# Kernel tuning notes

Hardware: AMD Instinct MI355X
Metric: run time of the kernel (lower is better)

## Reference

```python
import jax, jax.numpy as jnp
import numpy as np

B, T, C = 4, 2048, 1024
H = 16
D = C // H  # head_dim = 64


def setup_inputs() -> dict:
    key = jax.random.key(0)
    k1, k2, k3, k4, k5 = jax.random.split(key, 5)
    s = 0.02
    return {
        "x": jax.random.normal(k1, (B, T, C), dtype=jnp.float32),
        "W_qkv": jax.random.normal(k2, (C, 3 * C), dtype=jnp.float32) * s,
        "b_qkv": jax.random.normal(k3, (3 * C,), dtype=jnp.float32) * s,
        "W_o": jax.random.normal(k4, (C, C), dtype=jnp.float32) * s,
        "b_o": jax.random.normal(k5, (C,), dtype=jnp.float32) * s,
    }


def reference(x, W_qkv, b_qkv, W_o, b_o):
    b, t, c = x.shape
    scaling = D ** (-0.5)
    qkv = x @ W_qkv + b_qkv                      # [B,T,3C]
    q, k, v = jnp.split(qkv, 3, axis=-1)         # each [B,T,C]
    q = q.reshape(b, t, H, D).transpose(0, 2, 1, 3)  # [B,H,T,D]
    k = k.reshape(b, t, H, D).transpose(0, 2, 1, 3)
    v = v.reshape(b, t, H, D).transpose(0, 2, 1, 3)
    scores = jnp.einsum("bhqd,bhkd->bhqk", q, k) * scaling  # [B,H,T,T]
    mask = jnp.tril(jnp.ones((t, t), dtype=bool))            # causal
    scores = jnp.where(mask[None, None, :, :], scores, -jnp.inf)
    probs = jax.nn.softmax(scores, axis=-1)
    out = jnp.einsum("bhqk,bhkd->bhqd", probs, v)            # [B,H,T,D]
    out = out.transpose(0, 2, 1, 3).reshape(b, t, c)         # [B,T,C]
    return out @ W_o + b_o
```

## Files before the change

### kernel.cpp

```cpp
#include <hip/hip_runtime.h>
#include <hip/hip_bf16.h>

typedef unsigned short ushort_t;
typedef __attribute__((ext_vector_type(8))) short short8;
typedef __attribute__((ext_vector_type(4))) float floatx4;
typedef __attribute__((ext_vector_type(2))) unsigned uint2v;
typedef __attribute__((ext_vector_type(4))) unsigned uint4v;

#define B_ 4
#define T_ 2048
#define C_ 1024
#define H_ 16
#define D_ 64
#define BT_ (B_ * T_)
#define N3C (3 * C_)

#define KSC 0.18033688011112042f

__device__ __forceinline__ ushort_t f2bf(float f) {
    unsigned u = __float_as_uint(f);
    u += 0x7FFF + ((u >> 16) & 1);
    return (ushort_t)(u >> 16);
}
__device__ __forceinline__ unsigned pack2bf(float a, float b) {
    __hip_bfloat162 h = __float22bfloat162_rn(make_float2(a, b));
    return *(unsigned*)&h;
}

__device__ __forceinline__ void gload16(const ushort_t* g, ushort_t* l) {
    __builtin_amdgcn_global_load_lds((const __attribute__((address_space(1))) void*)g,
                                     (__attribute__((address_space(3))) void*)l, 16, 0, 0);
}

__global__ void convert_x_k(const float* __restrict__ xin, ushort_t* __restrict__ xb) {
    size_t i = ((size_t)blockIdx.x * 256 + threadIdx.x) * 8;
    const float* xf = xin + i;
    float4 a = *(const float4*)xf;
    float4 b = *(const float4*)(xf + 4);
    short8 o;
    o[0] = (short)f2bf(a.x); o[1] = (short)f2bf(a.y);
    o[2] = (short)f2bf(a.z); o[3] = (short)f2bf(a.w);
    o[4] = (short)f2bf(b.x); o[5] = (short)f2bf(b.y);
    o[6] = (short)f2bf(b.z); o[7] = (short)f2bf(b.w);
    *(short8*)&xb[i] = o;
}

__global__ void transpose_k(const float* __restrict__ in, ushort_t* __restrict__ out,
                            int R, int Nc) {
    __shared__ ushort_t t[32][33];
    int bc = blockIdx.x * 32;
    int br = blockIdx.y * 32;
    int lx = threadIdx.x & 31, ly = threadIdx.x >> 5;
#pragma unroll
    for (int i = 0; i < 4; ++i) {
        int r = ly + i * 8;
        t[r][lx] = f2bf(in[(size_t)(br + r) * Nc + bc + lx]);
    }
    __syncthreads();
#pragma unroll
    for (int i = 0; i < 4; ++i) {
        int r = ly + i * 8;
        out[(size_t)(bc + r) * R + br + lx] = t[lx][r];
    }
}

__global__ void vtrans_k(const ushort_t* __restrict__ in, ushort_t* __restrict__ out) {
    __shared__ ushort_t t[32][33];
    int bh = blockIdx.z;
    const ushort_t* I = in + (size_t)bh * T_ * D_;
    ushort_t* O = out + (size_t)bh * D_ * T_;
    int bt = blockIdx.x * 32, bd = blockIdx.y * 32;
    int lx = threadIdx.x & 31, ly = threadIdx.x >> 5;
#pragma unroll
    for (int i = 0; i < 4; ++i) {
        int r = ly + i * 8;
        t[r][lx] = I[(size_t)(bt + r) * D_ + bd + lx];
    }
    __syncthreads();
#pragma unroll
    for (int i = 0; i < 4; ++i) {
        int r = ly + i * 8;
        O[(size_t)(bd + r) * T_ + bt + lx] = t[lx][r];
    }
}

template <int MODE>
__launch_bounds__(256)
__global__ void gemm_bt(const ushort_t* __restrict__ A, const ushort_t* __restrict__ Bt,
                        const float* __restrict__ bias, float* __restrict__ Cout,
                        ushort_t* __restrict__ Qo, ushort_t* __restrict__ Ko,
                        ushort_t* __restrict__ Vo, int M, int N, int K) {
    __shared__ __align__(16) ushort_t Alds[128 * 32];
    __shared__ __align__(16) ushort_t Blds[128 * 32];
    int tid = threadIdx.x;
    int wave = tid >> 6, lane = tid & 63;
    int bm = blockIdx.x * 128, bn = blockIdx.y * 128;
    int wr = (wave >> 1) * 64, wc = (wave & 1) * 64;
    int lm = lane & 15, lk = (lane >> 4) * 8, lq = lane >> 4;

    floatx4 acc[4][4] = {};

    int srow = tid >> 2;
    int scol = (tid & 3) * 8;
    const ushort_t* Ab = A + (size_t)(bm + srow) * K + scol;
    const ushort_t* Bb = Bt + (size_t)(bn + srow) * K + scol;
    ushort_t* Al0 = &Alds[wave * 512];
    ushort_t* Al1 = &Alds[2048 + wave * 512];
    ushort_t* Bl0 = &Blds[wave * 512];
    ushort_t* Bl1 = &Blds[2048 + wave * 512];
    size_t rowskip = (size_t)64 * K;

    for (int k0 = 0; k0 < K; k0 += 32) {
        __syncthreads();
        gload16(Ab + k0, Al0);
        gload16(Ab + k0 + rowskip, Al1);
        gload16(Bb + k0, Bl0);
        gload16(Bb + k0 + rowskip, Bl1);
        __syncthreads();
        short8 af[4], bf[4];
#pragma unroll
        for (int i = 0; i < 4; ++i)
            af[i] = *(const short8*)&Alds[(wr + i * 16 + lm) * 32 + lk];
#pragma unroll
        for (int i = 0; i < 4; ++i)
            bf[i] = *(const short8*)&Blds[(wc + i * 16 + lm) * 32 + lk];
#pragma unroll
        for (int mi = 0; mi < 4; ++mi)
#pragma unroll
            for (int ni = 0; ni < 4; ++ni)
                acc[mi][ni] = __builtin_amdgcn_mfma_f32_16x16x32_bf16(
                    af[mi], bf[ni], acc[mi][ni], 0, 0, 0);
    }

#pragma unroll
    for (int mi = 0; mi < 4; ++mi) {
#pragma unroll
        for (int ni = 0; ni < 4; ++ni) {
            int col = bn + wc + ni * 16 + lm;
            float bv = bias[col];
#pragma unroll
            for (int r = 0; r < 4; ++r) {
                int row = bm + wr + mi * 16 + lq * 4 + r;
                float v = acc[mi][ni][r] + bv;
                if (MODE == 0) {
                    Cout[(size_t)row * N + col] = v;
                } else {
                    int b = row >> 11, t = row & (T_ - 1);
                    int which = col >> 10, c = col & (C_ - 1);
                    int h = c >> 6, d = c & 63;
                    int bh = b * H_ + h;
                    size_t idx = ((size_t)bh * T_ + t) * D_ + d;
                    if (which == 0)
                        Qo[idx] = f2bf(v * KSC);
                    else if (which == 1)
                        Ko[idx] = f2bf(v);
                    else
                        Vo[idx] = f2bf(v);
                }
            }
        }
    }
}

__launch_bounds__(256)
__global__ void attn_k(const ushort_t* __restrict__ Q, const ushort_t* __restrict__ K,
                       const ushort_t* __restrict__ Vt, ushort_t* __restrict__ O) {
    __shared__ __align__(16) ushort_t KV[2][2][64 * 64];

    int tid = threadIdx.x, wave = tid >> 6, lane = tid & 63;
    int id = blockIdx.x;
    int xcd = id & 7, j = id >> 3;
    int band = 31 - (j & 31);
    int bh = xcd + 8 * (j >> 5);
    int b = bh >> 4, h = bh & 15;
    int lm = lane & 15, lq = lane >> 4, m7 = lane & 7;

    const ushort_t* Qp = Q + (size_t)bh * T_ * D_;
    const ushort_t* Kp = K + (size_t)bh * T_ * D_;
    const ushort_t* Vp = Vt + (size_t)bh * D_ * T_;
    ushort_t* Ob = O + ((size_t)b * T_) * C_ + h * D_;

    int sr = lane >> 3;
    int sc = (lane & 7) ^ sr;
    const ushort_t* Kst = Kp + (size_t)(wave * 16 + sr) * D_ + sc * 8;
    const ushort_t* Vst = Vp + (size_t)(wave * 16 + sr) * T_ + sc * 8;
    int lds0 = (wave * 2 + 0) * 512;
    int lds1 = (wave * 2 + 1) * 512;

    short8 onesf = {};
    if (lm == 0) {
#pragma unroll
        for (int jj = 0; jj < 8; ++jj) onesf[jj] = (short)0x3F80;
    }

    int m0 = band * 64 + wave * 16;

    short8 qf0 = *(const short8*)&Qp[(size_t)(m0 + lm) * D_ + lq * 8];
    short8 qf1 = *(const short8*)&Qp[(size_t)(m0 + lm) * D_ + 32 + lq * 8];

    floatx4 oacc[5] = {};

    int ntw = band + 1;

    gload16(Kst, &KV[0][0][lds0]);
    gload16(Kst + (size_t)8 * D_, &KV[0][0][lds1]);
    gload16(Vst, &KV[0][1][lds0]);
    gload16(Vst + (size_t)8 * T_, &KV[0][1][lds1]);
    __syncthreads();

    int cur = 0;
    for (int it = 0; it < ntw; ++it) {
        if (it + 1 < ntw) {
            size_t kv0n = (size_t)(it + 1) * 64;
            gload16(Kst + kv0n * D_, &KV[cur ^ 1][0][lds0]);
            gload16(Kst + kv0n * D_ + 8 * D_, &KV[cur ^ 1][0][lds1]);
            gload16(Vst + kv0n, &KV[cur ^ 1][1][lds0]);
            gload16(Vst + kv0n + 8 * T_, &KV[cur ^ 1][1][lds1]);
        }
        const ushort_t* Kb = &KV[cur][0][0];
        const ushort_t* Vb = &KV[cur][1][0];

        short8 kf[4][2], vf[4][2];
#pragma unroll
        for (int nt = 0; nt < 4; ++nt) {
            kf[nt][0] = *(const short8*)&Kb[(nt * 16 + lm) * 64 + ((lq ^ m7) * 8)];
            kf[nt][1] = *(const short8*)&Kb[(nt * 16 + lm) * 64 + (((lq + 4) ^ m7) * 8)];
        }

        floatx4 st[4] = {};
#pragma unroll
        for (int nt = 0; nt < 4; ++nt) {
            st[nt] = __builtin_amdgcn_mfma_f32_16x16x32_bf16(kf[nt][0], qf0, st[nt], 0, 0, 0);
            st[nt] = __builtin_amdgcn_mfma_f32_16x16x32_bf16(kf[nt][1], qf1, st[nt], 0, 0, 0);
        }

#pragma unroll
        for (int dt = 0; dt < 4; ++dt) {
            vf[dt][0] = *(const short8*)&Vb[(dt * 16 + lm) * 64 + ((lq ^ m7) * 8)];
            vf[dt][1] = *(const short8*)&Vb[(dt * 16 + lm) * 64 + (((lq + 4) ^ m7) * 8)];
        }

        int kv0 = it * 64;
        if (it == ntw - 1) {
            int mg = m0 + lm;
#pragma unroll
            for (int nt = 0; nt < 4; ++nt)
#pragma unroll
                for (int r = 0; r < 4; ++r) {
                    int kvg = kv0 + nt * 16 + lq * 4 + r;
                    if (kvg > mg) st[nt][r] = -__builtin_inff();
                }
        }

        unsigned e0 = pack2bf(__builtin_amdgcn_exp2f(st[0][0]), __builtin_amdgcn_exp2f(st[0][1]));
        unsigned e1 = pack2bf(__builtin_amdgcn_exp2f(st[0][2]), __builtin_amdgcn_exp2f(st[0][3]));
        unsigned e2 = pack2bf(__builtin_amdgcn_exp2f(st[1][0]), __builtin_amdgcn_exp2f(st[1][1]));
        unsigned e3 = pack2bf(__builtin_amdgcn_exp2f(st[1][2]), __builtin_amdgcn_exp2f(st[1][3]));
        unsigned e4 = pack2bf(__builtin_amdgcn_exp2f(st[2][0]), __builtin_amdgcn_exp2f(st[2][1]));
        unsigned e5 = pack2bf(__builtin_amdgcn_exp2f(st[2][2]), __builtin_amdgcn_exp2f(st[2][3]));
        unsigned e6 = pack2bf(__builtin_amdgcn_exp2f(st[3][0]), __builtin_amdgcn_exp2f(st[3][1]));
        unsigned e7 = pack2bf(__builtin_amdgcn_exp2f(st[3][2]), __builtin_amdgcn_exp2f(st[3][3]));

        uint2v ra = __builtin_amdgcn_permlane32_swap(e0, e2, false, false);
        uint2v wa = __builtin_amdgcn_permlane16_swap(ra[0], ra[1], false, false);
        uint2v rb = __builtin_amdgcn_permlane32_swap(e1, e3, false, false);
        uint2v wb = __builtin_amdgcn_permlane16_swap(rb[0], rb[1], false, false);
        uint2v rc = __builtin_amdgcn_permlane32_swap(e4, e6, false, false);
        uint2v wc = __builtin_amdgcn_permlane16_swap(rc[0], rc[1], false, false);
        uint2v rd = __builtin_amdgcn_permlane32_swap(e5, e7, false, false);
        uint2v wd = __builtin_amdgcn_permlane16_swap(rd[0], rd[1], false, false);

        short8 pb0 = __builtin_bit_cast(short8, (uint4v){wa[0], wb[0], wa[1], wb[1]});
        short8 pb1 = __builtin_bit_cast(short8, (uint4v){wc[0], wd[0], wc[1], wd[1]});

#pragma unroll
        for (int dt = 0; dt < 4; ++dt) {
            oacc[dt] = __builtin_amdgcn_mfma_f32_16x16x32_bf16(vf[dt][0], pb0, oacc[dt], 0, 0, 0);
            oacc[dt] = __builtin_amdgcn_mfma_f32_16x16x32_bf16(vf[dt][1], pb1, oacc[dt], 0, 0, 0);
        }
        oacc[4] = __builtin_amdgcn_mfma_f32_16x16x32_bf16(onesf, pb0, oacc[4], 0, 0, 0);
        oacc[4] = __builtin_amdgcn_mfma_f32_16x16x32_bf16(onesf, pb1, oacc[4], 0, 0, 0);

        __syncthreads();
        cur ^= 1;
    }

    float li = __shfl(oacc[4][0], lm, 64);
    float inv = 1.0f / li;
    int tg = m0 + lm;
#pragma unroll
    for (int dt = 0; dt < 4; ++dt) {
        uint2 pk;
        pk.x = pack2bf(oacc[dt][0] * inv, oacc[dt][1] * inv);
        pk.y = pack2bf(oacc[dt][2] * inv, oacc[dt][3] * inv);
        *(uint2*)&Ob[(size_t)tg * C_ + dt * 16 + lq * 4] = pk;
    }
}

extern "C" void kernel_launch(void* const* d_in, const int* in_sizes, int n_in,
                              void* d_out, int out_size, void* d_ws, size_t ws_size,
                              hipStream_t stream) {
    const float* x    = (const float*)d_in[0];
    const float* Wqkv = (const float*)d_in[1];
    const float* bqkv = (const float*)d_in[2];
    const float* Wo   = (const float*)d_in[3];
    const float* bo   = (const float*)d_in[4];

    ushort_t* ws = (ushort_t*)d_ws;
    ushort_t* WqkvT = ws;
    ushort_t* WoT   = WqkvT + (size_t)N3C * C_;
    ushort_t* Xb    = WoT + (size_t)C_ * C_;
    ushort_t* Qs    = Xb + (size_t)BT_ * C_;
    ushort_t* Ks    = Qs + (size_t)BT_ * C_;
    ushort_t* Vs    = Ks + (size_t)BT_ * C_;
    ushort_t* Attn  = Vs + (size_t)BT_ * C_;

    convert_x_k<<<BT_ * C_ / (256 * 8), 256, 0, stream>>>(x, Xb);
    transpose_k<<<dim3(N3C / 32, C_ / 32), 256, 0, stream>>>(Wqkv, WqkvT, C_, N3C);
    transpose_k<<<dim3(C_ / 32, C_ / 32), 256, 0, stream>>>(Wo, WoT, C_, C_);
    gemm_bt<1><<<dim3(BT_ / 128, N3C / 128), 256, 0, stream>>>(
        Xb, WqkvT, bqkv, nullptr, Qs, Ks, Attn, BT_, N3C, C_);
    vtrans_k<<<dim3(T_ / 32, D_ / 32, B_ * H_), 256, 0, stream>>>(Attn, Vs);
    attn_k<<<2048, 256, 0, stream>>>(Qs, Ks, Vs, Attn);
    gemm_bt<0><<<dim3(BT_ / 128, C_ / 128), 256, 0, stream>>>(
        Attn, WoT, bo, (float*)d_out, nullptr, nullptr, nullptr, BT_, C_, C_);
}
```

Measured before the change: 278.9 us.

## Fuse prep kernels, double-buffer GEMM LDS, write V transposed, add MFMA priority

Merges the x conversion and the two weight transposes into one launch, and removes the separate V transpose kernel by having the QKV GEMM epilogue write V directly in [bh][d][t] layout. The GEMM main loop now double-buffers its LDS tiles so global-to-LDS loads for the next k-step overlap the current MFMAs, at the cost of twice the LDS. The attention kernel raises wave priority around its MFMA blocks with s_setprio. The transposed V store is strided in t, which may make the epilogue writes less coalesced.

```diff
diff --git a/kernel.cpp b/kernel.cpp
--- a/kernel.cpp
+++ b/kernel.cpp
@@ -32,24 +32,32 @@
                                      (__attribute__((address_space(3))) void*)l, 16, 0, 0);
 }
 
-__global__ void convert_x_k(const float* __restrict__ xin, ushort_t* __restrict__ xb) {
-    size_t i = ((size_t)blockIdx.x * 256 + threadIdx.x) * 8;
-    const float* xf = xin + i;
-    float4 a = *(const float4*)xf;
-    float4 b = *(const float4*)(xf + 4);
-    short8 o;
-    o[0] = (short)f2bf(a.x); o[1] = (short)f2bf(a.y);
-    o[2] = (short)f2bf(a.z); o[3] = (short)f2bf(a.w);
-    o[4] = (short)f2bf(b.x); o[5] = (short)f2bf(b.y);
-    o[6] = (short)f2bf(b.z); o[7] = (short)f2bf(b.w);
-    *(short8*)&xb[i] = o;
-}
-
-__global__ void transpose_k(const float* __restrict__ in, ushort_t* __restrict__ out,
-                            int R, int Nc) {
+__global__ void prep_k(const float* __restrict__ x, ushort_t* __restrict__ xb,
+                       const float* __restrict__ Wqkv, ushort_t* __restrict__ WqkvT,
+                       const float* __restrict__ Wo, ushort_t* __restrict__ WoT) {
     __shared__ ushort_t t[32][33];
-    int bc = blockIdx.x * 32;
-    int br = blockIdx.y * 32;
+    int id = blockIdx.x;
+    if (id < 4096) {
+        size_t i = ((size_t)id * 256 + threadIdx.x) * 8;
+        const float* xf = x + i;
+        float4 a = *(const float4*)xf;
+        float4 b = *(const float4*)(xf + 4);
+        short8 o;
+        o[0] = (short)f2bf(a.x); o[1] = (short)f2bf(a.y);
+        o[2] = (short)f2bf(a.z); o[3] = (short)f2bf(a.w);
+        o[4] = (short)f2bf(b.x); o[5] = (short)f2bf(b.y);
+        o[6] = (short)f2bf(b.z); o[7] = (short)f2bf(b.w);
+        *(short8*)&xb[i] = o;
+        return;
+    }
+    int tt = id - 4096;
+    int bx = tt & 127, by = tt >> 7;
+    const float* in;
+    ushort_t* out;
+    int Nc, bc;
+    if (bx < 96) { in = Wqkv; out = WqkvT; Nc = N3C; bc = bx * 32; }
+    else         { in = Wo;   out = WoT;   Nc = C_;  bc = (bx - 96) * 32; }
+    int br = by * 32;
     int lx = threadIdx.x & 31, ly = threadIdx.x >> 5;
 #pragma unroll
     for (int i = 0; i < 4; ++i) {
@@ -60,27 +68,7 @@
 #pragma unroll
     for (int i = 0; i < 4; ++i) {
         int r = ly + i * 8;
-        out[(size_t)(bc + r) * R + br + lx] = t[lx][r];
-    }
-}
-
-__global__ void vtrans_k(const ushort_t* __restrict__ in, ushort_t* __restrict__ out) {
-    __shared__ ushort_t t[32][33];
-    int bh = blockIdx.z;
-    const ushort_t* I = in + (size_t)bh * T_ * D_;
-    ushort_t* O = out + (size_t)bh * D_ * T_;
-    int bt = blockIdx.x * 32, bd = blockIdx.y * 32;
-    int lx = threadIdx.x & 31, ly = threadIdx.x >> 5;
-#pragma unroll
-    for (int i = 0; i < 4; ++i) {
-        int r = ly + i * 8;
-        t[r][lx] = I[(size_t)(bt + r) * D_ + bd + lx];
-    }
-    __syncthreads();
-#pragma unroll
-    for (int i = 0; i < 4; ++i) {
-        int r = ly + i * 8;
-        O[(size_t)(bd + r) * T_ + bt + lx] = t[lx][r];
+        out[(size_t)(bc + r) * C_ + br + lx] = t[lx][r];
     }
 }
 
@@ -90,8 +78,8 @@
                         const float* __restrict__ bias, float* __restrict__ Cout,
                         ushort_t* __restrict__ Qo, ushort_t* __restrict__ Ko,
                         ushort_t* __restrict__ Vo, int M, int N, int K) {
-    __shared__ __align__(16) ushort_t Alds[128 * 32];
-    __shared__ __align__(16) ushort_t Blds[128 * 32];
+    __shared__ __align__(16) ushort_t Alds[2][128 * 32];
+    __shared__ __align__(16) ushort_t Blds[2][128 * 32];
     int tid = threadIdx.x;
     int wave = tid >> 6, lane = tid & 63;
     int bm = blockIdx.x * 128, bn = blockIdx.y * 128;
@@ -104,32 +92,38 @@
     int scol = (tid & 3) * 8;
     const ushort_t* Ab = A + (size_t)(bm + srow) * K + scol;
     const ushort_t* Bb = Bt + (size_t)(bn + srow) * K + scol;
-    ushort_t* Al0 = &Alds[wave * 512];
-    ushort_t* Al1 = &Alds[2048 + wave * 512];
-    ushort_t* Bl0 = &Blds[wave * 512];
-    ushort_t* Bl1 = &Blds[2048 + wave * 512];
+    int lo0 = wave * 512, lo1 = 2048 + wave * 512;
     size_t rowskip = (size_t)64 * K;
 
+    gload16(Ab, &Alds[0][lo0]);
+    gload16(Ab + rowskip, &Alds[0][lo1]);
+    gload16(Bb, &Blds[0][lo0]);
+    gload16(Bb + rowskip, &Blds[0][lo1]);
+    __syncthreads();
+
+    int cur = 0;
     for (int k0 = 0; k0 < K; k0 += 32) {
-        __syncthreads();
-        gload16(Ab + k0, Al0);
-        gload16(Ab + k0 + rowskip, Al1);
-        gload16(Bb + k0, Bl0);
-        gload16(Bb + k0 + rowskip, Bl1);
-        __syncthreads();
+        if (k0 + 32 < K) {
+            gload16(Ab + k0 + 32, &Alds[cur ^ 1][lo0]);
+            gload16(Ab + k0 + 32 + rowskip, &Alds[cur ^ 1][lo1]);
+            gload16(Bb + k0 + 32, &Blds[cur ^ 1][lo0]);
+            gload16(Bb + k0 + 32 + rowskip, &Blds[cur ^ 1][lo1]);
+        }
         short8 af[4], bf[4];
 #pragma unroll
         for (int i = 0; i < 4; ++i)
-            af[i] = *(const short8*)&Alds[(wr + i * 16 + lm) * 32 + lk];
+            af[i] = *(const short8*)&Alds[cur][(wr + i * 16 + lm) * 32 + lk];
 #pragma unroll
         for (int i = 0; i < 4; ++i)
-            bf[i] = *(const short8*)&Blds[(wc + i * 16 + lm) * 32 + lk];
+            bf[i] = *(const short8*)&Blds[cur][(wc + i * 16 + lm) * 32 + lk];
 #pragma unroll
         for (int mi = 0; mi < 4; ++mi)
 #pragma unroll
             for (int ni = 0; ni < 4; ++ni)
                 acc[mi][ni] = __builtin_amdgcn_mfma_f32_16x16x32_bf16(
                     af[mi], bf[ni], acc[mi][ni], 0, 0, 0);
+        __syncthreads();
+        cur ^= 1;
     }
 
 #pragma unroll
@@ -149,13 +143,12 @@
                     int which = col >> 10, c = col & (C_ - 1);
                     int h = c >> 6, d = c & 63;
                     int bh = b * H_ + h;
-                    size_t idx = ((size_t)bh * T_ + t) * D_ + d;
                     if (which == 0)
-                        Qo[idx] = f2bf(v * KSC);
+                        Qo[((size_t)bh * T_ + t) * D_ + d] = f2bf(v * KSC);
                     else if (which == 1)
-                        Ko[idx] = f2bf(v);
+                        Ko[((size_t)bh * T_ + t) * D_ + d] = f2bf(v);
                     else
-                        Vo[idx] = f2bf(v);
+                        Vo[((size_t)bh * D_ + d) * T_ + t] = f2bf(v);
                 }
             }
         }
@@ -228,11 +221,13 @@
         }
 
         floatx4 st[4] = {};
+        __builtin_amdgcn_s_setprio(1);
 #pragma unroll
         for (int nt = 0; nt < 4; ++nt) {
             st[nt] = __builtin_amdgcn_mfma_f32_16x16x32_bf16(kf[nt][0], qf0, st[nt], 0, 0, 0);
             st[nt] = __builtin_amdgcn_mfma_f32_16x16x32_bf16(kf[nt][1], qf1, st[nt], 0, 0, 0);
         }
+        __builtin_amdgcn_s_setprio(0);
 
 #pragma unroll
         for (int dt = 0; dt < 4; ++dt) {
@@ -273,6 +268,7 @@
         short8 pb0 = __builtin_bit_cast(short8, (uint4v){wa[0], wb[0], wa[1], wb[1]});
         short8 pb1 = __builtin_bit_cast(short8, (uint4v){wc[0], wd[0], wc[1], wd[1]});
 
+        __builtin_amdgcn_s_setprio(1);
 #pragma unroll
         for (int dt = 0; dt < 4; ++dt) {
             oacc[dt] = __builtin_amdgcn_mfma_f32_16x16x32_bf16(vf[dt][0], pb0, oacc[dt], 0, 0, 0);
@@ -280,6 +276,7 @@
         }
         oacc[4] = __builtin_amdgcn_mfma_f32_16x16x32_bf16(onesf, pb0, oacc[4], 0, 0, 0);
         oacc[4] = __builtin_amdgcn_mfma_f32_16x16x32_bf16(onesf, pb1, oacc[4], 0, 0, 0);
+        __builtin_amdgcn_s_setprio(0);
 
         __syncthreads();
         cur ^= 1;
@@ -315,12 +312,9 @@
     ushort_t* Vs    = Ks + (size_t)BT_ * C_;
     ushort_t* Attn  = Vs + (size_t)BT_ * C_;
 
-    convert_x_k<<<BT_ * C_ / (256 * 8), 256, 0, stream>>>(x, Xb);
-    transpose_k<<<dim3(N3C / 32, C_ / 32), 256, 0, stream>>>(Wqkv, WqkvT, C_, N3C);
-    transpose_k<<<dim3(C_ / 32, C_ / 32), 256, 0, stream>>>(Wo, WoT, C_, C_);
+    prep_k<<<8192, 256, 0, stream>>>(x, Xb, Wqkv, WqkvT, Wo, WoT);
     gemm_bt<1><<<dim3(BT_ / 128, N3C / 128), 256, 0, stream>>>(
-        Xb, WqkvT, bqkv, nullptr, Qs, Ks, Attn, BT_, N3C, C_);
-    vtrans_k<<<dim3(T_ / 32, D_ / 32, B_ * H_), 256, 0, stream>>>(Attn, Vs);
+        Xb, WqkvT, bqkv, nullptr, Qs, Ks, Vs, BT_, N3C, C_);
     attn_k<<<2048, 256, 0, stream>>>(Qs, Ks, Vs, Attn);
     gemm_bt<0><<<dim3(BT_ / 128, C_ / 128), 256, 0, stream>>>(
         Attn, WoT, bo, (float*)d_out, nullptr, nullptr, nullptr, BT_, C_, C_);
```

Measured after the change: 269.2 us. -3.5%, faster.
